# Kernel tuning notes

Measured on AMD Instinct MI355X. Metric: run time of the kernel, lower is better.

The kernel has to match this reference:

```python
import jax, jax.numpy as jnp
import numpy as np

N_TYPES = 4
D_DESC = 256
H = 256
N_ATOMS = 131072


def setup_inputs() -> dict:
    key = jax.random.key(0)
    ks = jax.random.split(key, 8)
    descriptors = jax.random.normal(ks[0], (N_ATOMS, D_DESC), dtype=jnp.float32)
    elems = jax.random.randint(ks[1], (N_ATOMS,), 0, N_TYPES, dtype=jnp.int32)
    # Per-type MLP params: stacked over the type axis T.
    s1 = 1.0 / np.sqrt(D_DESC)
    s2 = 1.0 / np.sqrt(H)
    W1 = jax.random.normal(ks[2], (N_TYPES, D_DESC, H), dtype=jnp.float32) * s1
    b1 = jnp.zeros((N_TYPES, H), dtype=jnp.float32)
    W2 = jax.random.normal(ks[3], (N_TYPES, H, H), dtype=jnp.float32) * s2
    b2 = jnp.zeros((N_TYPES, H), dtype=jnp.float32)
    W3 = jax.random.normal(ks[4], (N_TYPES, H), dtype=jnp.float32) * s2  # output dim 1, squeezed
    b3 = jnp.zeros((N_TYPES,), dtype=jnp.float32)
    return {"descriptors": descriptors, "elems": elems,
            "W1": W1, "b1": b1, "W2": W2, "b2": b2, "W3": W3, "b3": b3}


def reference(descriptors, elems, W1, b1, W2, b2, W3, b3):
    # Equivalent to: for each atom, run the MLP subnet of its element type and
    # scatter the scalar output back to the per-atom attribute vector.
    # Vectorized as batched-per-type GEMMs followed by a per-atom type gather
    # (dense dispatch: fixed shapes, jit-friendly).
    # h1: [T, N, H]
    h1 = jnp.tanh(jnp.einsum('nd,tdh->tnh', descriptors, W1) + b1[:, None, :])
    h2 = jnp.tanh(jnp.einsum('tnh,thk->tnk', h1, W2) + b2[:, None, :])
    out_t = jnp.einsum('tnh,th->tn', h2, W3) + b3[:, None]  # [T, N]
    # select per-atom row according to its element type
    per_atom = out_t[elems, jnp.arange(out_t.shape[1])]  # [N]
    return per_atom
```

## Files before the change

kernel.cpp:

```cpp
#include <hip/hip_runtime.h>
#include <hip/hip_bf16.h>
#include <stdint.h>


typedef __attribute__((ext_vector_type(8))) short short8;
typedef __attribute__((ext_vector_type(4))) float f32x4;

#define NPB 256
#define NTY 4

typedef __attribute__((address_space(3))) void lds_void;
typedef __attribute__((address_space(1))) const void glb_void;

__device__ __forceinline__ unsigned short f2bf(float f) {
    union { float f; uint32_t u; } v; v.f = f;
    uint32_t u = v.u;
    uint32_t r = (u + 0x7FFFu + ((u >> 16) & 1u)) >> 16;
    return (unsigned short)r;
}
__device__ __forceinline__ float fast_tanh(float x) {
    x = fminf(fmaxf(x, -10.0f), 10.0f);
    float e = __expf(2.0f * x);
    return (e - 1.0f) * __builtin_amdgcn_rcpf(e + 1.0f);
}


__global__ void count_k(const int* __restrict__ elems, int n, int chunk,
                        int* __restrict__ counts) {
    __shared__ int h[NTY];
    if (threadIdx.x < NTY) h[threadIdx.x] = 0;
    __syncthreads();
    const int start = blockIdx.x * chunk;
    const int end   = min(start + chunk, n);
    for (int i = start + threadIdx.x; i < end; i += blockDim.x)
        atomicAdd(&h[elems[i]], 1);
    __syncthreads();
    if (threadIdx.x < NTY) counts[threadIdx.x * NPB + blockIdx.x] = h[threadIdx.x];
}

__global__ void prefix_k(const int* __restrict__ counts,
                         int* __restrict__ cursor, int* __restrict__ hdr) {
    __shared__ int tot[NTY];
    const int t = threadIdx.x;
    if (t < NTY) {
        int s = 0;
        for (int b = 0; b < NPB; ++b) s += counts[t * NPB + b];
        tot[t] = s;
    }
    __syncthreads();
    if (t == 0) {
        int b = 0, tb = 0;
        for (int ty = 0; ty < NTY; ++ty) {
            hdr[ty]      = tot[ty];
            hdr[8 + ty]  = b;
            hdr[12 + ty] = tb;
            b  += tot[ty];
            tb += (tot[ty] + 63) >> 6;
        }
        hdr[16] = tb;
    }
    __syncthreads();
    if (t < NTY) {
        int run = hdr[8 + t];
        for (int b = 0; b < NPB; ++b) {
            cursor[t * NPB + b] = run;
            run += counts[t * NPB + b];
        }
    }
}

__global__ void scatter_k(const int* __restrict__ elems, int n, int chunk,
                          const int* __restrict__ cursor, int* __restrict__ sorted) {
    __shared__ int cur[NTY];
    if (threadIdx.x < NTY) cur[threadIdx.x] = cursor[threadIdx.x * NPB + blockIdx.x];
    __syncthreads();
    const int start = blockIdx.x * chunk;
    const int end   = min(start + chunk, n);
    for (int i = start + threadIdx.x; i < end; i += blockDim.x) {
        int ty  = elems[i];
        int pos = atomicAdd(&cur[ty], 1);
        sorted[pos] = i;
    }
}

__global__ void wconv_k(const float* __restrict__ W1, const float* __restrict__ W2,
                        unsigned short* __restrict__ w1s, unsigned short* __restrict__ w2s) {
    int gid  = blockIdx.x * blockDim.x + threadIdx.x;
    int lane = gid & 63;
    int ks   = (gid >> 6) & 7;
    int tile = (gid >> 9) & 15;
    int t    = (gid >> 13) & 3;
    int layer = gid >> 15;
    const float* W = layer ? W2 : W1;
    unsigned short* o = layer ? w2s : w1s;
    int dbase = ks * 32 + ((lane >> 4) << 3);
    int col   = tile * 16 + (lane & 15);
    unsigned short v[8];
#pragma unroll
    for (int j = 0; j < 8; ++j)
        v[j] = f2bf(W[(size_t)t * 65536 + (size_t)(dbase + j) * 256 + col]);
    unsigned short* dst = o + ((size_t)(t * 16 + tile) * 8 + ks) * 512 + lane * 8;
    *(short8*)dst = *(short8*)v;
}

#define TILEINFO(TL, T, CNT, BASE, AST)                          \
    {                                                            \
        T = 3;                                                   \
        if      ((TL) < hdr[13]) T = 0;                          \
        else if ((TL) < hdr[14]) T = 1;                          \
        else if ((TL) < hdr[15]) T = 2;                          \
        CNT = hdr[T]; BASE = hdr[8 + T];                         \
        AST = ((TL) - hdr[12 + T]) * 64;                         \
    }

__global__ __launch_bounds__(256, 2) void mlp1_k(
    const float* __restrict__ desc,
    const float* __restrict__ b1g,
    const int* __restrict__ hdr,
    const int* __restrict__ sorted,
    const unsigned short* __restrict__ w1s,
    unsigned short* __restrict__ h1g)
{
    __shared__ __align__(16) char buf[32768];

    const int tid  = threadIdx.x;
    const int lane = tid & 63;
    const int w    = tid >> 6;

    const int b = blockIdx.x;
    if (b >= hdr[16]) return;
    int t, cnt, base, astart;
    TILEINFO(b, t, cnt, base, astart);

    {
        const int slot = tid >> 2;
        const int q4   = tid & 3;
        const int gg   = astart + slot;
        const int idx  = (gg < cnt) ? sorted[base + gg] : 0;
        const float4* row = (const float4*)(desc + (size_t)idx * 256);
#pragma unroll
        for (int i = 0; i < 16; ++i) {
            const int f = q4 + i * 4;
            const float4 v = row[f];
            unsigned short h4[4];
            h4[0] = f2bf(v.x); h4[1] = f2bf(v.y);
            h4[2] = f2bf(v.z); h4[3] = f2bf(v.w);
            const int off = slot * 512 + ((f * 8) ^ ((slot & 7) << 4));
            *(ushort4*)(buf + off) = *(ushort4*)h4;
        }
    }
    __syncthreads();

    const unsigned short* w1t = w1s + (size_t)t * (16 * 8 * 512);

    f32x4 acc[4][4];
#pragma unroll
    for (int q = 0; q < 4; ++q)
#pragma unroll
        for (int nt = 0; nt < 4; ++nt)
            acc[q][nt] = (f32x4){0.f, 0.f, 0.f, 0.f};

#pragma unroll
    for (int ks = 0; ks < 8; ++ks) {
        short8 af[4];
#pragma unroll
        for (int q = 0; q < 4; ++q)
            af[q] = *(const short8*)(w1t + ((size_t)((w * 4 + q) * 8 + ks)) * 512 + lane * 8);
        short8 bh[4];
        const int colb = ks * 64 + ((lane >> 4) << 4);
#pragma unroll
        for (int nt = 0; nt < 4; ++nt) {
            const int row = nt * 16 + (lane & 15);
            const int off = row * 512 + (colb ^ ((row & 7) << 4));
            bh[nt] = *(const short8*)(buf + off);
        }
#pragma unroll
        for (int q = 0; q < 4; ++q)
#pragma unroll
            for (int nt = 0; nt < 4; ++nt)
                acc[q][nt] = __builtin_amdgcn_mfma_f32_16x16x32_bf16(af[q], bh[nt], acc[q][nt], 0, 0, 0);
    }
    __syncthreads();

#pragma unroll
    for (int q = 0; q < 4; ++q) {
        const int h0 = (w * 4 + q) * 16 + ((lane >> 4) << 2);
        const float4 bb = *(const float4*)(b1g + t * 256 + h0);
#pragma unroll
        for (int nt = 0; nt < 4; ++nt) {
            const int atom = nt * 16 + (lane & 15);
            unsigned short h4[4];
            h4[0] = f2bf(fast_tanh(acc[q][nt][0] + bb.x));
            h4[1] = f2bf(fast_tanh(acc[q][nt][1] + bb.y));
            h4[2] = f2bf(fast_tanh(acc[q][nt][2] + bb.z));
            h4[3] = f2bf(fast_tanh(acc[q][nt][3] + bb.w));
            const int off = atom * 512 + ((h0 * 2) ^ ((atom & 7) << 4));
            *(ushort4*)(buf + off) = *(ushort4*)h4;
        }
    }
    __syncthreads();

    {
        const int p  = tid & 31;
        const int a0 = tid >> 5;
#pragma unroll
        for (int i = 0; i < 8; ++i) {
            const int atom = a0 + i * 8;
            const int gg   = astart + atom;
            const uint4 v = *(const uint4*)(buf + atom * 512 + ((p * 16) ^ ((atom & 7) << 4)));
            if (gg < cnt)
                *(uint4*)((char*)h1g + (size_t)(base + gg) * 512 + p * 16) = v;
        }
    }
}

__global__ __launch_bounds__(256, 2) void mlp2_k(
    const float* __restrict__ b2g,
    const float* __restrict__ W3,
    const float* __restrict__ b3,
    const int* __restrict__ hdr,
    const int* __restrict__ sorted,
    const unsigned short* __restrict__ w2s,
    const unsigned short* __restrict__ h1g,
    float* __restrict__ out)
{
    __shared__ __align__(16) char buf[32768];
    __shared__ float part[4][64];

    const int tid  = threadIdx.x;
    const int lane = tid & 63;
    const int w    = tid >> 6;

    const int b = blockIdx.x;
    if (b >= hdr[16]) return;
    int t, cnt, base, astart;
    TILEINFO(b, t, cnt, base, astart);

#pragma unroll
    for (int i = 0; i < 8; ++i) {
        const int row = w * 16 + i * 2 + (lane >> 5);
        const int p   = lane & 31;
        const int gg  = astart + row;
        const size_t srow = (size_t)(base + ((gg < cnt) ? gg : 0));
        const char* src = (const char*)h1g + srow * 512 + ((p * 16) ^ ((row & 7) << 4));
        char* dst = buf + w * 8192 + i * 1024;
        __builtin_amdgcn_global_load_lds((glb_void*)src, (lds_void*)dst, 16, 0, 0);
    }
    asm volatile("s_waitcnt vmcnt(0)" ::: "memory");
    __syncthreads();

    const unsigned short* w2t = w2s + (size_t)t * (16 * 8 * 512);

    f32x4 acc2[4][4];
#pragma unroll
    for (int mt = 0; mt < 4; ++mt)
#pragma unroll
        for (int q = 0; q < 4; ++q)
            acc2[mt][q] = (f32x4){0.f, 0.f, 0.f, 0.f};

#pragma unroll
    for (int ks = 0; ks < 8; ++ks) {
        short8 bw[4];
#pragma unroll
        for (int q = 0; q < 4; ++q)
            bw[q] = *(const short8*)(w2t + ((size_t)((w * 4 + q) * 8 + ks)) * 512 + lane * 8);
        short8 ah[4];
        const int colb = ks * 64 + ((lane >> 4) << 4);
#pragma unroll
        for (int mt = 0; mt < 4; ++mt) {
            const int row = mt * 16 + (lane & 15);
            const int off = row * 512 + (colb ^ ((row & 7) << 4));
            ah[mt] = *(const short8*)(buf + off);
        }
#pragma unroll
        for (int mt = 0; mt < 4; ++mt)
#pragma unroll
            for (int q = 0; q < 4; ++q)
                acc2[mt][q] = __builtin_amdgcn_mfma_f32_16x16x32_bf16(ah[mt], bw[q], acc2[mt][q], 0, 0, 0);
    }

    float psum[4][4];
#pragma unroll
    for (int mt = 0; mt < 4; ++mt)
#pragma unroll
        for (int r = 0; r < 4; ++r)
            psum[mt][r] = 0.f;

#pragma unroll
    for (int q = 0; q < 4; ++q) {
        const int kout = (w * 4 + q) * 16 + (lane & 15);
        const float w3v = W3[t * 256 + kout];
        const float b2v = b2g[t * 256 + kout];
#pragma unroll
        for (int mt = 0; mt < 4; ++mt)
#pragma unroll
            for (int r = 0; r < 4; ++r)
                psum[mt][r] += fast_tanh(acc2[mt][q][r] + b2v) * w3v;
    }
#pragma unroll
    for (int m = 1; m <= 8; m <<= 1)
#pragma unroll
        for (int mt = 0; mt < 4; ++mt)
#pragma unroll
            for (int r = 0; r < 4; ++r)
                psum[mt][r] += __shfl_xor(psum[mt][r], m, 64);

    if ((lane & 15) == 0) {
        const int gq = lane >> 4;
#pragma unroll
        for (int mt = 0; mt < 4; ++mt)
#pragma unroll
            for (int r = 0; r < 4; ++r)
                part[w][mt * 16 + gq * 4 + r] = psum[mt][r];
    }
    __syncthreads();

    if (tid < 64) {
        const int gg = astart + tid;
        if (gg < cnt) {
            float v = part[0][tid] + part[1][tid] + part[2][tid] + part[3][tid] + b3[t];
            out[sorted[base + gg]] = v;
        }
    }
}

extern "C" void kernel_launch(void* const* d_in, const int* in_sizes, int n_in,
                              void* d_out, int out_size, void* d_ws, size_t ws_size,
                              hipStream_t stream) {
    const float* desc = (const float*)d_in[0];
    const int*   elems = (const int*)d_in[1];
    const float* W1 = (const float*)d_in[2];
    const float* b1 = (const float*)d_in[3];
    const float* W2 = (const float*)d_in[4];
    const float* b2 = (const float*)d_in[5];
    const float* W3 = (const float*)d_in[6];
    const float* b3 = (const float*)d_in[7];
    float* out = (float*)d_out;
    const int n = in_sizes[1];

    char* ws = (char*)d_ws;
    int* hdr    = (int*)ws;
    int* counts = (int*)(ws + 128);
    int* cursor = (int*)(ws + 128 + 4 * NPB * 4);
    int* sorted = (int*)(ws + 128 + 8 * NPB * 4);
    unsigned short* w1s = (unsigned short*)((char*)sorted + (size_t)n * 4);
    unsigned short* w2s = w1s + (size_t)4 * 16 * 8 * 512;
    unsigned short* h1g = w2s + (size_t)4 * 16 * 8 * 512;

    const int chunk = (n + NPB - 1) / NPB;

    count_k<<<NPB, 256, 0, stream>>>(elems, n, chunk, counts);
    prefix_k<<<1, 64, 0, stream>>>(counts, cursor, hdr);
    scatter_k<<<NPB, 256, 0, stream>>>(elems, n, chunk, cursor, sorted);
    wconv_k<<<256, 256, 0, stream>>>(W1, W2, w1s, w2s);

    const int maxtiles = (n >> 6) + 4;
    mlp1_k<<<maxtiles, 256, 0, stream>>>(desc, b1, hdr, sorted, w1s, h1g);
    mlp2_k<<<maxtiles, 256, 0, stream>>>(b2, W3, b3, hdr, sorted, w2s, h1g, out);
}
```

Measured before the change: 107.0 us.

## Load descriptor fragments directly from global into MFMA operands, skipping LDS staging

The layer-1 kernel no longer stages the gathered descriptor tile into shared memory. Each lane now reads its own descriptor row from global memory inside the k-loop, converts it to bf16 and feeds it straight to the MFMA, which removes two barriers and the LDS round trip. Launch bounds are raised from 2 to 4 blocks per multiprocessor to add occupancy for hiding the latency. The trade-off is that each wave now reads the same descriptor rows from global memory (four waves per block), and the lower register budget may cause spills.

```diff
diff --git a/kernel.cpp b/kernel.cpp
--- a/kernel.cpp
+++ b/kernel.cpp
@@ -113,7 +113,7 @@
         AST = ((TL) - hdr[12 + T]) * 64;                         \
     }
 
-__global__ __launch_bounds__(256, 2) void mlp1_k(
+__global__ __launch_bounds__(256, 4) void mlp1_k(
     const float* __restrict__ desc,
     const float* __restrict__ b1g,
     const int* __restrict__ hdr,
@@ -126,30 +126,21 @@
     const int tid  = threadIdx.x;
     const int lane = tid & 63;
     const int w    = tid >> 6;
+    const int g    = lane >> 4;
+    const int a16  = lane & 15;
 
     const int b = blockIdx.x;
     if (b >= hdr[16]) return;
     int t, cnt, base, astart;
     TILEINFO(b, t, cnt, base, astart);
 
-    {
-        const int slot = tid >> 2;
-        const int q4   = tid & 3;
-        const int gg   = astart + slot;
-        const int idx  = (gg < cnt) ? sorted[base + gg] : 0;
-        const float4* row = (const float4*)(desc + (size_t)idx * 256);
-#pragma unroll
-        for (int i = 0; i < 16; ++i) {
-            const int f = q4 + i * 4;
-            const float4 v = row[f];
-            unsigned short h4[4];
-            h4[0] = f2bf(v.x); h4[1] = f2bf(v.y);
-            h4[2] = f2bf(v.z); h4[3] = f2bf(v.w);
-            const int off = slot * 512 + ((f * 8) ^ ((slot & 7) << 4));
-            *(ushort4*)(buf + off) = *(ushort4*)h4;
-        }
-    }
-    __syncthreads();
+    const float* rowp[4];
+#pragma unroll
+    for (int nt = 0; nt < 4; ++nt) {
+        const int gg  = astart + nt * 16 + a16;
+        const int idx = (gg < cnt) ? sorted[base + gg] : 0;
+        rowp[nt] = desc + (size_t)idx * 256;
+    }
 
     const unsigned short* w1t = w1s + (size_t)t * (16 * 8 * 512);
 
@@ -167,12 +158,17 @@
         for (int q = 0; q < 4; ++q)
             af[q] = *(const short8*)(w1t + ((size_t)((w * 4 + q) * 8 + ks)) * 512 + lane * 8);
         short8 bh[4];
-        const int colb = ks * 64 + ((lane >> 4) << 4);
+        const int e0 = ks * 32 + g * 8;
 #pragma unroll
         for (int nt = 0; nt < 4; ++nt) {
-            const int row = nt * 16 + (lane & 15);
-            const int off = row * 512 + (colb ^ ((row & 7) << 4));
-            bh[nt] = *(const short8*)(buf + off);
+            const float4 v0 = *(const float4*)(rowp[nt] + e0);
+            const float4 v1 = *(const float4*)(rowp[nt] + e0 + 4);
+            union { short8 s; __hip_bfloat162 h[4]; } u;
+            u.h[0] = __float22bfloat162_rn(make_float2(v0.x, v0.y));
+            u.h[1] = __float22bfloat162_rn(make_float2(v0.z, v0.w));
+            u.h[2] = __float22bfloat162_rn(make_float2(v1.x, v1.y));
+            u.h[3] = __float22bfloat162_rn(make_float2(v1.z, v1.w));
+            bh[nt] = u.s;
         }
 #pragma unroll
         for (int q = 0; q < 4; ++q)
@@ -180,15 +176,14 @@
             for (int nt = 0; nt < 4; ++nt)
                 acc[q][nt] = __builtin_amdgcn_mfma_f32_16x16x32_bf16(af[q], bh[nt], acc[q][nt], 0, 0, 0);
     }
-    __syncthreads();
 
 #pragma unroll
     for (int q = 0; q < 4; ++q) {
-        const int h0 = (w * 4 + q) * 16 + ((lane >> 4) << 2);
+        const int h0 = (w * 4 + q) * 16 + (g << 2);
         const float4 bb = *(const float4*)(b1g + t * 256 + h0);
 #pragma unroll
         for (int nt = 0; nt < 4; ++nt) {
-            const int atom = nt * 16 + (lane & 15);
+            const int atom = nt * 16 + a16;
             unsigned short h4[4];
             h4[0] = f2bf(fast_tanh(acc[q][nt][0] + bb.x));
             h4[1] = f2bf(fast_tanh(acc[q][nt][1] + bb.y));
```

Result: slower. 148.0 us (+38.4%).
